# Performance work log

Measured on AMD Instinct MI355X. Metric: run time of the kernel, lower is better.

Reference implementation:

```python
import jax, jax.numpy as jnp
import numpy as np

N_NODES = 50000
N_EDGES = 800000
NUM_FEATURES = 128
HIDDEN = 256
OUT = 64


def setup_inputs() -> dict:
    key = jax.random.key(0)
    k1, k2, k3, k4 = jax.random.split(key, 4)
    x = jax.random.normal(k1, (N_NODES, NUM_FEATURES), dtype=jnp.float32)
    # Glorot-ish scaled weights
    W1 = jax.random.normal(k2, (NUM_FEATURES, HIDDEN), dtype=jnp.float32) * (1.0 / np.sqrt(NUM_FEATURES))
    b1 = jnp.zeros((HIDDEN,), dtype=jnp.float32)
    W2 = jax.random.normal(k3, (HIDDEN, OUT), dtype=jnp.float32) * (1.0 / np.sqrt(HIDDEN))
    b2 = jnp.zeros((OUT,), dtype=jnp.float32)
    edge_index = jax.random.randint(k4, (2, N_EDGES), 0, N_NODES, dtype=jnp.int64)
    return {"x": x, "W1": W1, "b1": b1, "W2": W2, "b2": b2,
            "edge_index": edge_index, "batch_size": 2, "pred_steps": 12}


def _gcn_conv(x, W, b, row, col, n):
    """PyG-style GCNConv: x' = D^-1/2 (A + I) D^-1/2 (x W) + b.
    row/col already include self-loops."""
    deg = jax.ops.segment_sum(jnp.ones_like(row, dtype=x.dtype), row, num_segments=n)
    dinv = jnp.where(deg > 0, deg ** -0.5, 0.0)
    norm = dinv[row] * dinv[col]          # [E+N]
    h = x @ W                              # transform first (in < out irrelevant here)
    msg = h[col] * norm[:, None]           # gather + scale: [E+N, d_out]
    agg = jax.ops.segment_sum(msg, row, num_segments=n)  # scatter-add
    return agg + b


def reference(x, W1, b1, W2, b2, edge_index, batch_size, pred_steps):
    n = x.shape[0]
    loops = jnp.arange(n, dtype=edge_index.dtype)
    row = jnp.concatenate([edge_index[0], loops])  # add self-loops once, reused by both convs
    col = jnp.concatenate([edge_index[1], loops])

    h = jax.nn.relu(_gcn_conv(x, W1, b1, row, col, n))
    # F.dropout in eval mode is identity (inference baseline)
    h = _gcn_conv(h, W2, b2, row, col, n)
    h = jax.nn.log_softmax(h, axis=1)      # [N, OUT]
    # unsqueeze/expand/repeat -> [batch_size, pred_steps, N, OUT]
    out = jnp.broadcast_to(h[None, None, :, :], (batch_size, pred_steps, n, h.shape[1]))
    return out
```

## Files before the change

kernel.cpp:

```cpp
#include <hip/hip_runtime.h>

__global__ __launch_bounds__(256) void hist_rows(const int* __restrict__ row, int* __restrict__ cnt, int E) {
    int e = blockIdx.x * 256 + threadIdx.x;
    if (e < E) atomicAdd(&cnt[row[e]], 1);
}

__global__ __launch_bounds__(256) void alloc_buckets(const int* __restrict__ cnt,
                                                     int* __restrict__ base, int* __restrict__ fill,
                                                     float* __restrict__ dinv,
                                                     int* __restrict__ total, int n) {
    int i = blockIdx.x * 256 + threadIdx.x;
    if (i >= n) return;
    int c = cnt[i];
    int b = atomicAdd(total, c);
    base[i] = b;
    fill[i] = b;
    dinv[i] = rsqrtf(1.0f + (float)c);
}

__global__ __launch_bounds__(256) void fill_buckets(const int* __restrict__ row, const int* __restrict__ col,
                                                    int* __restrict__ fill, int* __restrict__ cols, int E) {
    int e = blockIdx.x * 256 + threadIdx.x;
    if (e < E) {
        int pos = atomicAdd(&fill[row[e]], 1);
        cols[pos] = col[e];
    }
}

__global__ __launch_bounds__(256) void agg_x(const float* __restrict__ x,
                                             const int* __restrict__ base, const int* __restrict__ cnt,
                                             const int* __restrict__ cols, const float* __restrict__ dinv,
                                             float* __restrict__ AGGX, int n) {
    int w = (blockIdx.x * 256 + threadIdx.x) >> 6;
    int lane = threadIdx.x & 63;
    if (w >= n) return;
    float di = dinv[w];
    float2 xv = ((const float2*)(x + (size_t)w * 128))[lane];
    float2 acc = make_float2(xv.x * di * di, xv.y * di * di);
    int b0 = base[w], deg = cnt[w];
    for (int s = 0; s < deg; s += 64) {
        int seg = min(64, deg - s);
        int myc = 0; float myd = 0.f;
        if (lane < seg) { myc = cols[b0 + s + lane]; myd = dinv[myc]; }
        for (int j = 0; j < seg; ++j) {
            int c = __shfl(myc, j, 64);
            float nrm = di * __shfl(myd, j, 64);
            float2 v = ((const float2*)(x + (size_t)c * 128))[lane];
            acc.x = fmaf(v.x, nrm, acc.x);
            acc.y = fmaf(v.y, nrm, acc.y);
        }
    }
    ((float2*)(AGGX + (size_t)w * 128))[lane] = acc;
}

__global__ __launch_bounds__(256) void agg_h2(const float* __restrict__ H2,
                                              const int* __restrict__ base, const int* __restrict__ cnt,
                                              const int* __restrict__ cols, const float* __restrict__ dinv,
                                              const float* __restrict__ b2,
                                              float* __restrict__ AGG2, int n) {
    int w = (blockIdx.x * 256 + threadIdx.x) >> 6;
    int lane = threadIdx.x & 63;
    if (w >= n) return;
    float di = dinv[w];
    float acc = H2[(size_t)w * 64 + lane] * di * di;
    int b0 = base[w], deg = cnt[w];
    for (int s = 0; s < deg; s += 64) {
        int seg = min(64, deg - s);
        int myc = 0; float myd = 0.f;
        if (lane < seg) { myc = cols[b0 + s + lane]; myd = dinv[myc]; }
        for (int j = 0; j < seg; ++j) {
            int c = __shfl(myc, j, 64);
            float nrm = di * __shfl(myd, j, 64);
            acc = fmaf(H2[(size_t)c * 64 + lane], nrm, acc);
        }
    }
    AGG2[(size_t)w * 64 + lane] = acc + b2[lane];
}

__global__ __launch_bounds__(256) void gemm64(const float* __restrict__ A,
                                              const float* __restrict__ B,
                                              const float* __restrict__ bias,
                                              float* __restrict__ C,
                                              int M, int N, int K, int relu) {
    __shared__ float As[32][65];
    __shared__ float Bs[32][65];
    const int bm = blockIdx.x * 64;
    const int bn = blockIdx.y * 64;
    const int tid = threadIdx.x;
    const int tx = tid & 15;
    const int ty = tid >> 4;
    float acc[4][4] = {};

    for (int k0 = 0; k0 < K; k0 += 32) {
        #pragma unroll
        for (int i = 0; i < 8; ++i) {
            int t = tid + i * 256;
            int r = t >> 5, c = t & 31;
            int gr = bm + r;
            float v = 0.f;
            if (gr < M) v = A[(size_t)gr * K + k0 + c];
            As[c][r] = v;
        }
        #pragma unroll
        for (int i = 0; i < 8; ++i) {
            int t = tid + i * 256;
            int r = t >> 6, c = t & 63;
            Bs[r][c] = B[(size_t)(k0 + r) * N + bn + c];
        }
        __syncthreads();
        #pragma unroll
        for (int k = 0; k < 32; ++k) {
            float av[4], bv[4];
            #pragma unroll
            for (int u = 0; u < 4; ++u) av[u] = As[k][ty * 4 + u];
            #pragma unroll
            for (int u = 0; u < 4; ++u) bv[u] = Bs[k][tx * 4 + u];
            #pragma unroll
            for (int i2 = 0; i2 < 4; ++i2)
                #pragma unroll
                for (int j = 0; j < 4; ++j)
                    acc[i2][j] = fmaf(av[i2], bv[j], acc[i2][j]);
        }
        __syncthreads();
    }
    float bv4[4];
    #pragma unroll
    for (int j = 0; j < 4; ++j) bv4[j] = bias ? bias[bn + tx * 4 + j] : 0.f;
    #pragma unroll
    for (int i2 = 0; i2 < 4; ++i2) {
        int gr = bm + ty * 4 + i2;
        if (gr < M) {
            float4 o;
            o.x = acc[i2][0] + bv4[0];
            o.y = acc[i2][1] + bv4[1];
            o.z = acc[i2][2] + bv4[2];
            o.w = acc[i2][3] + bv4[3];
            if (relu) {
                o.x = fmaxf(o.x, 0.f); o.y = fmaxf(o.y, 0.f);
                o.z = fmaxf(o.z, 0.f); o.w = fmaxf(o.w, 0.f);
            }
            *(float4*)(C + (size_t)gr * N + bn + tx * 4) = o;
        }
    }
}

__global__ __launch_bounds__(256) void final_out(const float* __restrict__ AGG2,
                                                 float* __restrict__ out, int n, int copies) {
    int w = (blockIdx.x * 256 + threadIdx.x) >> 6;
    int lane = threadIdx.x & 63;
    if (w >= n) return;
    size_t idx = (size_t)w * 64 + lane;
    float v = AGG2[idx];
    float m = v;
    #pragma unroll
    for (int off = 32; off > 0; off >>= 1) m = fmaxf(m, __shfl_xor(m, off, 64));
    float e = expf(v - m);
    float s = e;
    #pragma unroll
    for (int off = 32; off > 0; off >>= 1) s += __shfl_xor(s, off, 64);
    float res = v - m - logf(s);
    size_t stride = (size_t)n * 64;
    for (int c = 0; c < copies; ++c) out[(size_t)c * stride + idx] = res;
}

extern "C" void kernel_launch(void* const* d_in, const int* in_sizes, int n_in,
                              void* d_out, int out_size, void* d_ws, size_t ws_size,
                              hipStream_t stream) {
    const float* x  = (const float*)d_in[0];
    const float* W1 = (const float*)d_in[1];
    const float* b1 = (const float*)d_in[2];
    const float* W2 = (const float*)d_in[3];
    const float* b2 = (const float*)d_in[4];
    const int*   ei = (const int*)d_in[5];

    const int n = in_sizes[0] / 128;
    const int E = in_sizes[5] / 2;
    float* out = (float*)d_out;
    const size_t stride = (size_t)n * 64;
    const int copies = (int)(out_size / stride);

    float* dinv  = out;
    int*   cnt   = (int*)(out + n);
    int*   base  = (int*)(out + 2 * (size_t)n);
    int*   fill  = (int*)(out + 3 * (size_t)n);
    int*   total = (int*)(out + 4 * (size_t)n);
    int*   cols  = (int*)(out + 1 * stride);
    float* AGGX  = out + 2 * stride;
    float* H1    = out + 4 * stride;
    float* H2    = out + 8 * stride;
    float* AGG2  = out + 9 * stride;

    hipMemsetAsync(cnt, 0, (3 * (size_t)n + 64) * sizeof(int), stream);

    hist_rows   <<<(E + 255) / 256, 256, 0, stream>>>(ei, cnt, E);
    alloc_buckets<<<(n + 255) / 256, 256, 0, stream>>>(cnt, base, fill, dinv, total, n);
    fill_buckets<<<(E + 255) / 256, 256, 0, stream>>>(ei, ei + E, fill, cols, E);

    agg_x<<<(n + 3) / 4, 256, 0, stream>>>(x, base, cnt, cols, dinv, AGGX, n);
    gemm64<<<dim3((n + 63) / 64, 4), 256, 0, stream>>>(AGGX, W1, b1, H1, n, 256, 128, 1);

    gemm64<<<dim3((n + 63) / 64, 1), 256, 0, stream>>>(H1, W2, nullptr, H2, n, 64, 256, 0);
    agg_h2<<<(n + 3) / 4, 256, 0, stream>>>(H2, base, cnt, cols, dinv, b2, AGG2, n);

    final_out<<<(n + 3) / 4, 256, 0, stream>>>(AGG2, out, n, copies);
}
```

Before: 710.6 us.

## Precompute edge norms in padded CSR buckets and unroll neighbor gathers by eight

Buckets are padded to multiples of eight and each edge entry now stores the neighbor index together with its precomputed normalization weight. Padding entries are zeroed so they add nothing. The aggregation kernels load eight edges at a time, issue eight independent row gathers, and split the sum over four accumulators to increase memory-level parallelism and drop the shuffles and dinv lookups. The GEMM shared-memory tiles are padded to 68 so rows can be read as float4. The cost is an extra memset of the padded edge buffer and some wasted gathers on padding entries.

```diff
diff --git a/kernel.cpp b/kernel.cpp
--- a/kernel.cpp
+++ b/kernel.cpp
@@ -12,69 +12,86 @@
     int i = blockIdx.x * 256 + threadIdx.x;
     if (i >= n) return;
     int c = cnt[i];
-    int b = atomicAdd(total, c);
+    int cp = (c + 7) & ~7;
+    int b = atomicAdd(total, cp);
     base[i] = b;
     fill[i] = b;
     dinv[i] = rsqrtf(1.0f + (float)c);
 }
 
 __global__ __launch_bounds__(256) void fill_buckets(const int* __restrict__ row, const int* __restrict__ col,
-                                                    int* __restrict__ fill, int* __restrict__ cols, int E) {
+                                                    int* __restrict__ fill, const float* __restrict__ dinv,
+                                                    int2* __restrict__ edge2, int E) {
     int e = blockIdx.x * 256 + threadIdx.x;
     if (e < E) {
-        int pos = atomicAdd(&fill[row[e]], 1);
-        cols[pos] = col[e];
+        int r = row[e], c = col[e];
+        int pos = atomicAdd(&fill[r], 1);
+        edge2[pos] = make_int2(c, __float_as_int(dinv[r] * dinv[c]));
     }
 }
 
 __global__ __launch_bounds__(256) void agg_x(const float* __restrict__ x,
                                              const int* __restrict__ base, const int* __restrict__ cnt,
-                                             const int* __restrict__ cols, const float* __restrict__ dinv,
+                                             const int2* __restrict__ edge2, const float* __restrict__ dinv,
                                              float* __restrict__ AGGX, int n) {
     int w = (blockIdx.x * 256 + threadIdx.x) >> 6;
     int lane = threadIdx.x & 63;
     if (w >= n) return;
     float di = dinv[w];
     float2 xv = ((const float2*)(x + (size_t)w * 128))[lane];
-    float2 acc = make_float2(xv.x * di * di, xv.y * di * di);
-    int b0 = base[w], deg = cnt[w];
-    for (int s = 0; s < deg; s += 64) {
-        int seg = min(64, deg - s);
-        int myc = 0; float myd = 0.f;
-        if (lane < seg) { myc = cols[b0 + s + lane]; myd = dinv[myc]; }
-        for (int j = 0; j < seg; ++j) {
-            int c = __shfl(myc, j, 64);
-            float nrm = di * __shfl(myd, j, 64);
-            float2 v = ((const float2*)(x + (size_t)c * 128))[lane];
-            acc.x = fmaf(v.x, nrm, acc.x);
-            acc.y = fmaf(v.y, nrm, acc.y);
-        }
-    }
-    ((float2*)(AGGX + (size_t)w * 128))[lane] = acc;
+    float2 a0 = make_float2(xv.x * di * di, xv.y * di * di);
+    float2 a1 = make_float2(0.f, 0.f), a2 = a1, a3 = a1;
+    const int2* eb = edge2 + base[w];
+    int dp = (cnt[w] + 7) & ~7;
+    for (int j = 0; j < dp; j += 8) {
+        int2 e[8];
+        #pragma unroll
+        for (int u = 0; u < 8; ++u) e[u] = eb[j + u];
+        float2 v[8];
+        #pragma unroll
+        for (int u = 0; u < 8; ++u)
+            v[u] = ((const float2*)(x + (size_t)e[u].x * 128))[lane];
+        #pragma unroll
+        for (int u = 0; u < 8; ++u) {
+            float nr = __int_as_float(e[u].y);
+            float2* a = (u & 3) == 0 ? &a0 : (u & 3) == 1 ? &a1 : (u & 3) == 2 ? &a2 : &a3;
+            a->x = fmaf(v[u].x, nr, a->x);
+            a->y = fmaf(v[u].y, nr, a->y);
+        }
+    }
+    float2 o = make_float2(a0.x + a1.x + a2.x + a3.x, a0.y + a1.y + a2.y + a3.y);
+    ((float2*)(AGGX + (size_t)w * 128))[lane] = o;
 }
 
 __global__ __launch_bounds__(256) void agg_h2(const float* __restrict__ H2,
                                               const int* __restrict__ base, const int* __restrict__ cnt,
-                                              const int* __restrict__ cols, const float* __restrict__ dinv,
+                                              const int2* __restrict__ edge2, const float* __restrict__ dinv,
                                               const float* __restrict__ b2,
                                               float* __restrict__ AGG2, int n) {
     int w = (blockIdx.x * 256 + threadIdx.x) >> 6;
     int lane = threadIdx.x & 63;
     if (w >= n) return;
     float di = dinv[w];
-    float acc = H2[(size_t)w * 64 + lane] * di * di;
-    int b0 = base[w], deg = cnt[w];
-    for (int s = 0; s < deg; s += 64) {
-        int seg = min(64, deg - s);
-        int myc = 0; float myd = 0.f;
-        if (lane < seg) { myc = cols[b0 + s + lane]; myd = dinv[myc]; }
-        for (int j = 0; j < seg; ++j) {
-            int c = __shfl(myc, j, 64);
-            float nrm = di * __shfl(myd, j, 64);
-            acc = fmaf(H2[(size_t)c * 64 + lane], nrm, acc);
-        }
-    }
-    AGG2[(size_t)w * 64 + lane] = acc + b2[lane];
+    float a0 = H2[(size_t)w * 64 + lane] * di * di;
+    float a1 = 0.f, a2 = 0.f, a3 = 0.f;
+    const int2* eb = edge2 + base[w];
+    int dp = (cnt[w] + 7) & ~7;
+    for (int j = 0; j < dp; j += 8) {
+        int2 e[8];
+        #pragma unroll
+        for (int u = 0; u < 8; ++u) e[u] = eb[j + u];
+        float v[8];
+        #pragma unroll
+        for (int u = 0; u < 8; ++u)
+            v[u] = H2[(size_t)e[u].x * 64 + lane];
+        #pragma unroll
+        for (int u = 0; u < 8; ++u) {
+            float nr = __int_as_float(e[u].y);
+            float* a = (u & 3) == 0 ? &a0 : (u & 3) == 1 ? &a1 : (u & 3) == 2 ? &a2 : &a3;
+            *a = fmaf(v[u], nr, *a);
+        }
+    }
+    AGG2[(size_t)w * 64 + lane] = a0 + a1 + a2 + a3 + b2[lane];
 }
 
 __global__ __launch_bounds__(256) void gemm64(const float* __restrict__ A,
@@ -82,8 +99,8 @@
                                               const float* __restrict__ bias,
                                               float* __restrict__ C,
                                               int M, int N, int K, int relu) {
-    __shared__ float As[32][65];
-    __shared__ float Bs[32][65];
+    __shared__ float As[32][68];
+    __shared__ float Bs[32][68];
     const int bm = blockIdx.x * 64;
     const int bn = blockIdx.y * 64;
     const int tid = threadIdx.x;
@@ -110,16 +127,15 @@
         __syncthreads();
         #pragma unroll
         for (int k = 0; k < 32; ++k) {
-            float av[4], bv[4];
-            #pragma unroll
-            for (int u = 0; u < 4; ++u) av[u] = As[k][ty * 4 + u];
-            #pragma unroll
-            for (int u = 0; u < 4; ++u) bv[u] = Bs[k][tx * 4 + u];
+            float4 av = *(const float4*)&As[k][ty * 4];
+            float4 bv = *(const float4*)&Bs[k][tx * 4];
+            float a4[4] = {av.x, av.y, av.z, av.w};
+            float b4[4] = {bv.x, bv.y, bv.z, bv.w};
             #pragma unroll
             for (int i2 = 0; i2 < 4; ++i2)
                 #pragma unroll
                 for (int j = 0; j < 4; ++j)
-                    acc[i2][j] = fmaf(av[i2], bv[j], acc[i2][j]);
+                    acc[i2][j] = fmaf(a4[i2], b4[j], acc[i2][j]);
         }
         __syncthreads();
     }
@@ -184,23 +200,24 @@
     int*   base  = (int*)(out + 2 * (size_t)n);
     int*   fill  = (int*)(out + 3 * (size_t)n);
     int*   total = (int*)(out + 4 * (size_t)n);
-    int*   cols  = (int*)(out + 1 * stride);
+    int2*  edge2 = (int2*)(out + 1 * stride);
     float* AGGX  = out + 2 * stride;
     float* H1    = out + 4 * stride;
     float* H2    = out + 8 * stride;
     float* AGG2  = out + 9 * stride;
 
     hipMemsetAsync(cnt, 0, (3 * (size_t)n + 64) * sizeof(int), stream);
-
-    hist_rows   <<<(E + 255) / 256, 256, 0, stream>>>(ei, cnt, E);
+    hipMemsetAsync(edge2, 0, ((size_t)E + 8 * (size_t)n) * sizeof(int2), stream);
+
+    hist_rows    <<<(E + 255) / 256, 256, 0, stream>>>(ei, cnt, E);
     alloc_buckets<<<(n + 255) / 256, 256, 0, stream>>>(cnt, base, fill, dinv, total, n);
-    fill_buckets<<<(E + 255) / 256, 256, 0, stream>>>(ei, ei + E, fill, cols, E);
-
-    agg_x<<<(n + 3) / 4, 256, 0, stream>>>(x, base, cnt, cols, dinv, AGGX, n);
+    fill_buckets <<<(E + 255) / 256, 256, 0, stream>>>(ei, ei + E, fill, dinv, edge2, E);
+
+    agg_x<<<(n + 3) / 4, 256, 0, stream>>>(x, base, cnt, edge2, dinv, AGGX, n);
     gemm64<<<dim3((n + 63) / 64, 4), 256, 0, stream>>>(AGGX, W1, b1, H1, n, 256, 128, 1);
 
     gemm64<<<dim3((n + 63) / 64, 1), 256, 0, stream>>>(H1, W2, nullptr, H2, n, 64, 256, 0);
-    agg_h2<<<(n + 3) / 4, 256, 0, stream>>>(H2, base, cnt, cols, dinv, b2, AGG2, n);
+    agg_h2<<<(n + 3) / 4, 256, 0, stream>>>(H2, base, cnt, edge2, dinv, b2, AGG2, n);
 
     final_out<<<(n + 3) / 4, 256, 0, stream>>>(AGG2, out, n, copies);
 }
```

Measured after the change: 610.9 us. -14.0%, faster.
